# Kernel tuning notes

Hardware: AMD Instinct MI355X
Metric: run time of the kernel (lower is better)

The kernel has to match this reference:

```python
import jax, jax.numpy as jnp
import numpy as np

B, N, D = 4, 2048, 1024
HEAD_DIMS = 128
NUM_HEADS = 8
PROJ = HEAD_DIMS * NUM_HEADS  # 1024


def setup_inputs() -> dict:
    key = jax.random.key(0)
    ks = jax.random.split(key, 5)
    # Weights stored as (in, out); xavier-normal-like scale
    def xavier(k, fan_in, fan_out):
        std = (2.0 / (fan_in + fan_out)) ** 0.5
        return jax.random.normal(k, (fan_in, fan_out), dtype=jnp.float32) * std
    return {
        "x": jax.random.normal(ks[0], (B, N, D), dtype=jnp.float32),
        "Wq": xavier(ks[1], D, PROJ),
        "Wk": xavier(ks[2], D, PROJ),
        "Wv": xavier(ks[3], D, PROJ),
        "Wo": xavier(ks[4], PROJ, PROJ),
    }


def reference(x, Wq, Wk, Wv, Wo):
    b, n, d = x.shape
    # QKV projections, split into heads: (b, h, n, hd)
    def split_heads(z):
        return z.reshape(b, n, NUM_HEADS, HEAD_DIMS).transpose(0, 2, 1, 3)
    q = split_heads(x @ Wq)
    k = split_heads(x @ Wk)
    v = split_heads(x @ Wv)
    scale = 1.0 / jnp.sqrt(jnp.float32(HEAD_DIMS))
    logits = jnp.einsum("bhqd,bhkd->bhqk", q, k) * scale
    weights = jax.nn.softmax(logits, axis=-1)
    out = jnp.einsum("bhqk,bhkd->bhqd", weights, v)
    out = out.transpose(0, 2, 1, 3).reshape(b, n, PROJ)
    return out @ Wo
```

## Files before the change

kernel.cpp:

```cpp
#include <hip/hip_runtime.h>
#include <hip/hip_bf16.h>


typedef __attribute__((ext_vector_type(8))) short short8;
typedef __attribute__((ext_vector_type(4))) short short4v;
typedef __attribute__((ext_vector_type(4))) float floatx4;
typedef __attribute__((ext_vector_type(8))) _Float16 half8;

#define MFMA_F16(a, b, c) __builtin_amdgcn_mfma_f32_16x16x32_f16( \
    __builtin_bit_cast(half8, (a)), __builtin_bit_cast(half8, (b)), (c), 0, 0, 0)

static constexpr int BATCH  = 4;
static constexpr int NHEADS = 8;
static constexpr int SEQ    = 2048;
static constexpr int HD     = 128;
static constexpr int DMODEL = 1024;
static constexpr int MROWS  = BATCH * SEQ;
static constexpr int NQKV   = 3 * DMODEL;

#define QSCALE2 0.12752283786512624f

static __device__ __forceinline__ short f16bits(float v) {
    return __builtin_bit_cast(short, (_Float16)v);
}

template <typename T>
static __device__ __forceinline__ short8 load8_f16(const T* p) {
    if constexpr (sizeof(T) == 2) {
        return *(const short8*)p;
    } else {
        const float4 f0 = *(const float4*)p;
        const float4 f1 = *(const float4*)(p + 4);
        short8 r;
        r[0] = f16bits(f0.x); r[1] = f16bits(f0.y);
        r[2] = f16bits(f0.z); r[3] = f16bits(f0.w);
        r[4] = f16bits(f1.x); r[5] = f16bits(f1.y);
        r[6] = f16bits(f1.z); r[7] = f16bits(f1.w);
        return r;
    }
}

static __device__ __forceinline__ void storeC(float* C, size_t idx, float v) {
    C[idx] = v;
}
static __device__ __forceinline__ void storeC(_Float16* C, size_t idx, float v) {
    C[idx] = (_Float16)v;
}

static __device__ __forceinline__ void gload16(const short* g, short* l) {
    __builtin_amdgcn_global_load_lds(
        (const __attribute__((address_space(1))) void*)g,
        (__attribute__((address_space(3))) void*)l, 16, 0, 0);
}

__global__ __launch_bounds__(256)
void prep(const float* __restrict__ x, short* __restrict__ xb,
          const float* __restrict__ W0, const float* __restrict__ W1,
          const float* __restrict__ W2, const float* __restrict__ W3,
          short* __restrict__ Wt, int K, int N)
{
    __shared__ short T[32][33];
    const int z = blockIdx.z;
    if (z >= 4) {
        const size_t chunk = ((size_t)(z - 4) * 1024 + blockIdx.y * 32 + blockIdx.x);
        const size_t i = (chunk * 256 + threadIdx.x) * 8;
        *(short8*)&xb[i] = load8_f16(&x[i]);
        return;
    }
    const float* W = (z == 0) ? W0 : (z == 1) ? W1 : (z == 2) ? W2 : W3;
    short* Wtz = Wt + (size_t)z * K * N;

    const int n0 = blockIdx.x * 32, k0 = blockIdx.y * 32;
    const int r = threadIdx.x >> 3, c4 = (threadIdx.x & 7) * 4;

    const float4 v = *(const float4*)&W[(size_t)(k0 + r) * N + n0 + c4];
    T[r][c4 + 0] = f16bits(v.x);
    T[r][c4 + 1] = f16bits(v.y);
    T[r][c4 + 2] = f16bits(v.z);
    T[r][c4 + 3] = f16bits(v.w);
    __syncthreads();

    short4v o;
    o[0] = T[c4 + 0][r]; o[1] = T[c4 + 1][r];
    o[2] = T[c4 + 2][r]; o[3] = T[c4 + 3][r];
    *(short4v*)&Wtz[(size_t)(n0 + r) * K + k0 + c4] = o;
}

__global__ __launch_bounds__(256)
void convx(const float* __restrict__ x, short* __restrict__ xb)
{
    const size_t i = ((size_t)blockIdx.x * 256 + threadIdx.x) * 8;
    *(short8*)&xb[i] = load8_f16(&x[i]);
}

__global__ __launch_bounds__(256)
void transpose_v(const short* __restrict__ V, short* __restrict__ Vt)
{
    __shared__ short T[64][72];
    const int s0 = blockIdx.x * 64;
    const int d0 = blockIdx.y * 64;
    const int bh = blockIdx.z;
    const short* Vi = V  + (size_t)bh * SEQ * HD;
    short*       Vo = Vt + (size_t)bh * HD * SEQ;

    const int r = threadIdx.x >> 3;
    const int c = threadIdx.x & 7;

    *(short8*)&T[r][c * 8]      = *(const short8*)&Vi[(size_t)(s0 + r) * HD + d0 + c * 8];
    *(short8*)&T[r + 32][c * 8] = *(const short8*)&Vi[(size_t)(s0 + r + 32) * HD + d0 + c * 8];
    __syncthreads();

    short8 o0, o1;
    #pragma unroll
    for (int j = 0; j < 8; ++j) {
        o0[j] = T[c * 8 + j][r];
        o1[j] = T[c * 8 + j][r + 32];
    }
    *(short8*)&Vo[(size_t)(d0 + r) * SEQ + s0 + c * 8]      = o0;
    *(short8*)&Vo[(size_t)(d0 + r + 32) * SEQ + s0 + c * 8] = o1;
}

template <typename OutT, bool QKV>
__global__ __launch_bounds__(256)
void gemm128(const short* __restrict__ A, const short* __restrict__ Bt,
             OutT* __restrict__ C, int M, int N, int K, size_t qkvStride)
{
    __shared__ __align__(16) short As[128 * 64];
    __shared__ __align__(16) short Bs[128 * 64];

    const int tid  = threadIdx.x;
    const int lane = tid & 63;
    const int w    = tid >> 6;
    const int quad = lane >> 4;
    const int l16  = lane & 15;

    const int m0 = blockIdx.x * 128;
    const int n0 = blockIdx.y * 128;
    const int wm = (w >> 1) * 64;
    const int wn = (w & 1) * 64;

    floatx4 acc[4][4] = {};

    const int srow   = tid >> 3;
    const int schunk = (tid & 7) ^ (srow & 7);
    const short* aG = A  + (size_t)(m0 + srow) * K + schunk * 8;
    const short* bG = Bt + (size_t)(n0 + srow) * K + schunk * 8;
    short* aL = As + tid * 8;
    short* bL = Bs + tid * 8;

    const int fsw = l16 & 7;

    for (int k0 = 0; k0 < K; k0 += 64) {
        __syncthreads();
        #pragma unroll
        for (int r = 0; r < 4; ++r) {
            gload16(aG + k0 + (size_t)(r * 32) * K, aL + r * 2048);
            gload16(bG + k0 + (size_t)(r * 32) * K, bL + r * 2048);
        }
        __syncthreads();

        #pragma unroll
        for (int kk = 0; kk < 2; ++kk) {
            short8 af[4], bf[4];
            #pragma unroll
            for (int mi = 0; mi < 4; ++mi)
                af[mi] = *(short8*)&As[(wm + mi * 16 + l16) * 64 +
                                       (((kk * 4 + quad) ^ fsw) * 8)];
            #pragma unroll
            for (int ni = 0; ni < 4; ++ni)
                bf[ni] = *(short8*)&Bs[(wn + ni * 16 + l16) * 64 +
                                       (((kk * 4 + quad) ^ fsw) * 8)];

            #pragma unroll
            for (int mi = 0; mi < 4; ++mi)
                #pragma unroll
                for (int ni = 0; ni < 4; ++ni)
                    acc[mi][ni] = MFMA_F16(af[mi], bf[ni], acc[mi][ni]);
        }
    }

    #pragma unroll
    for (int mi = 0; mi < 4; ++mi)
        #pragma unroll
        for (int ni = 0; ni < 4; ++ni)
            #pragma unroll
            for (int r = 0; r < 4; ++r) {
                const int m = m0 + wm + mi * 16 + quad * 4 + r;
                const int n = n0 + wn + ni * 16 + l16;
                float v = acc[mi][ni][r];
                if constexpr (QKV) {
                    const int qkv = n >> 10, rem = n & 1023;
                    const int h = rem >> 7, d = rem & 127;
                    const int b = m >> 11, s = m & 2047;
                    if (qkv == 0) v *= QSCALE2;
                    storeC(C, (size_t)qkv * qkvStride +
                              (((size_t)b * NHEADS + h) * SEQ + s) * HD + d, v);
                } else {
                    storeC(C, (size_t)m * N + n, v);
                }
            }
}

__global__ __launch_bounds__(128)
void attn_flash12(const short* __restrict__ Q, const short* __restrict__ K,
                  const short* __restrict__ Vt, _Float16* __restrict__ O)
{
    __shared__ __align__(16) short Ks[2][32 * 128];
    __shared__ __align__(16) short Vs[2][128 * 32];
    __shared__ __align__(16) short Plds[2][32 * 40];

    const int tid  = threadIdx.x;
    const int lane = tid & 63;
    const int w    = tid >> 6;
    const int quad = lane >> 4;
    const int l16  = lane & 15;

    const int h  = blockIdx.x & 7;
    const int qi = blockIdx.x >> 3;
    const int b  = blockIdx.y;
    const int q0 = qi * 64;

    const short* Qh  = Q  + (((size_t)b * NHEADS + h) * SEQ) * HD;
    const short* Kh  = K  + (((size_t)b * NHEADS + h) * SEQ) * HD;
    const short* Vth = Vt + (((size_t)b * NHEADS + h) * HD) * SEQ;

    short8 qf[2][4];
    #pragma unroll
    for (int mi = 0; mi < 2; ++mi) {
        const int qrow = q0 + w * 32 + mi * 16 + l16;
        #pragma unroll
        for (int c = 0; c < 4; ++c)
            qf[mi][c] = *(const short8*)&Qh[(size_t)qrow * HD + c * 32 + quad * 8];
    }

    const int kr0 = tid >> 4, kc0 = tid & 15;
    const short* kA0 = Kh + (size_t)kr0 * HD + ((kc0 ^ kr0) * 8);
    const short* kA1 = Kh + (size_t)(kr0 + 8) * HD + ((kc0 ^ (kr0 + 8)) * 8);
    const int vr0 = tid >> 2, vp0 = tid & 3;
    const short* vA = Vth + (size_t)vr0 * SEQ + ((vp0 ^ ((vr0 >> 1) & 3)) * 8);

    floatx4 acc[2][8] = {};
    floatx4 acc9[2] = {};

    short8 ones;
    #pragma unroll
    for (int j = 0; j < 8; ++j) ones[j] = 0x3C00;

    const int fswV = (l16 >> 1) & 3;
    short* Pw = &Plds[w][0];

    auto STAGE_K = [&](short* dst, int tile) {
        const size_t ko = (size_t)tile * 32 * HD;
        gload16(kA0 + ko,           dst + tid * 8);
        gload16(kA1 + ko,           dst + (tid + 128) * 8);
        gload16(kA0 + ko + 16 * HD, dst + (tid + 256) * 8);
        gload16(kA1 + ko + 16 * HD, dst + (tid + 384) * 8);
    };
    auto STAGE_V = [&](short* dst, int tile) {
        const size_t vo = (size_t)tile * 32;
        gload16(vA + vo,                      dst + tid * 8);
        gload16(vA + vo + (size_t)32 * SEQ,   dst + (tid + 128) * 8);
        gload16(vA + vo + (size_t)64 * SEQ,   dst + (tid + 256) * 8);
        gload16(vA + vo + (size_t)96 * SEQ,   dst + (tid + 384) * 8);
    };

    auto QK = [&](const short* Kb, floatx4 (&s)[2][2]) {
        #pragma unroll
        for (int c = 0; c < 4; ++c) {
            const int k_ = c * 4 + quad;
            short8 kf0 = *(short8*)&Kb[l16 * 128 + ((k_ ^ l16) * 8)];
            short8 kf1 = *(short8*)&Kb[(16 + l16) * 128 + ((k_ ^ l16) * 8)];
            #pragma unroll
            for (int mi = 0; mi < 2; ++mi) {
                s[mi][0] = MFMA_F16(qf[mi][c], kf0, s[mi][0]);
                s[mi][1] = MFMA_F16(qf[mi][c], kf1, s[mi][1]);
            }
        }
    };

    auto ITER = [&](int T, int BB, floatx4 (&sin)[2][2], floatx4 (&sout)[2][2]) {
        __syncthreads();
        if (T + 2 < SEQ / 32) STAGE_K(&Ks[BB][0], T + 2);
        if (T + 1 < SEQ / 32) STAGE_V(&Vs[BB ^ 1][0], T + 1);

        #pragma unroll
        for (int mi = 0; mi < 2; ++mi)
            #pragma unroll
            for (int r = 0; r < 4; ++r) {
                const float p0 = __builtin_amdgcn_exp2f(sin[mi][0][r]);
                const float p1 = __builtin_amdgcn_exp2f(sin[mi][1][r]);
                const int prow = mi * 16 + quad * 4 + r;
                Pw[prow * 40 + l16]      = f16bits(p0);
                Pw[prow * 40 + 16 + l16] = f16bits(p1);
            }

        #pragma unroll
        for (int mi = 0; mi < 2; ++mi) {
            sout[mi][0] = floatx4{};
            sout[mi][1] = floatx4{};
        }
        if (T + 1 < SEQ / 32) QK(&Ks[BB ^ 1][0], sout);

        short8 pf[2];
        #pragma unroll
        for (int mi = 0; mi < 2; ++mi) {
            pf[mi] = *(short8*)&Pw[(mi * 16 + l16) * 40 + quad * 8];
            acc9[mi] = MFMA_F16(pf[mi], ones, acc9[mi]);
        }
        const short* Vb = &Vs[BB][0];
        #pragma unroll
        for (int hc = 0; hc < 8; ++hc) {
            short8 vf = *(short8*)&Vb[(hc * 16 + l16) * 32 + ((quad ^ fswV) * 8)];
            #pragma unroll
            for (int mi = 0; mi < 2; ++mi)
                acc[mi][hc] = MFMA_F16(pf[mi], vf, acc[mi][hc]);
        }
    };

    STAGE_K(&Ks[0][0], 0);
    STAGE_V(&Vs[0][0], 0);
    STAGE_K(&Ks[1][0], 1);
    __syncthreads();
    floatx4 sc[2][2] = {}, sn[2][2];
    QK(&Ks[0][0], sc);

    for (int t = 0; t < SEQ / 32; t += 2) {
        ITER(t,     0, sc, sn);
        ITER(t + 1, 1, sn, sc);
    }

    #pragma unroll
    for (int mi = 0; mi < 2; ++mi) {
        float rinv[4];
        #pragma unroll
        for (int r = 0; r < 4; ++r)
            rinv[r] = 1.0f / fmaxf(acc9[mi][r], 1e-30f);
        #pragma unroll
        for (int hc = 0; hc < 8; ++hc)
            #pragma unroll
            for (int r = 0; r < 4; ++r) {
                const int row = q0 + w * 32 + mi * 16 + quad * 4 + r;
                O[((size_t)b * SEQ + row) * DMODEL + h * HD + hc * 16 + l16] =
                    (_Float16)(acc[mi][hc][r] * rinv[r]);
            }
    }
}

template <typename AT, typename OutT>
__global__ __launch_bounds__(256)
void gemm64(const AT* __restrict__ A, const float* __restrict__ W,
            OutT* __restrict__ C, int M, int N, int K, int headsplit)
{
    __shared__ __align__(16) short As[64][32];
    __shared__ __align__(16) short Bs[64][32];

    const int tid  = threadIdx.x;
    const int lane = tid & 63;
    const int w    = tid >> 6;
    const int quad = lane >> 4;
    const int l16  = lane & 15;

    const int m0 = blockIdx.x * 64;
    const int n0 = blockIdx.y * 64;
    const int wm = (w >> 1) * 32;
    const int wn = (w & 1) * 32;

    floatx4 acc[2][2] = {};

    const int arow = tid >> 2, acol = (tid & 3) * 8;
    const int brow = tid >> 3, bcol = (tid & 7) * 8;

    const AT*    aptr = A + (size_t)(m0 + arow) * K + acol;
    const float* bptr = W + (size_t)brow * N + n0 + bcol;

    for (int k0 = 0; k0 < K; k0 += 32) {
        short8 av = load8_f16(aptr + k0);
        short8 bv = load8_f16(bptr + (size_t)k0 * N);
        __syncthreads();
        *(short8*)&As[arow][acol] = av;
        #pragma unroll
        for (int j = 0; j < 8; ++j)
            Bs[bcol + j][brow] = bv[j];
        __syncthreads();

        short8 af0 = *(short8*)&As[wm + l16][quad * 8];
        short8 af1 = *(short8*)&As[wm + 16 + l16][quad * 8];
        short8 bf0 = *(short8*)&Bs[wn + l16][quad * 8];
        short8 bf1 = *(short8*)&Bs[wn + 16 + l16][quad * 8];

        acc[0][0] = MFMA_F16(af0, bf0, acc[0][0]);
        acc[0][1] = MFMA_F16(af0, bf1, acc[0][1]);
        acc[1][0] = MFMA_F16(af1, bf0, acc[1][0]);
        acc[1][1] = MFMA_F16(af1, bf1, acc[1][1]);
    }

    #pragma unroll
    for (int mi = 0; mi < 2; ++mi)
        #pragma unroll
        for (int ni = 0; ni < 2; ++ni)
            #pragma unroll
            for (int r = 0; r < 4; ++r) {
                const int m = m0 + wm + mi * 16 + quad * 4 + r;
                const int n = n0 + wn + ni * 16 + l16;
                const float v = acc[mi][ni][r];
                if (headsplit) {
                    const int b = m >> 11, nn = m & 2047;
                    const int h = n >> 7,  d  = n & 127;
                    storeC(C, (((size_t)b * NHEADS + h) * SEQ + nn) * HD + d, v);
                } else {
                    storeC(C, (size_t)m * N + n, v);
                }
            }
}

__global__ __launch_bounds__(256)
void attn_flash(const short* __restrict__ Q, const short* __restrict__ K,
                const short* __restrict__ V, _Float16* __restrict__ O)
{
    __shared__ __align__(16) short Ksf[32][136];
    __shared__ __align__(16) short Vtl[HD][40];
    __shared__ __align__(16) short Pldsf[4][16][40];

    const int tid  = threadIdx.x;
    const int lane = tid & 63;
    const int w    = tid >> 6;
    const int quad = lane >> 4;
    const int l16  = lane & 15;

    const int q0 = blockIdx.x * 64;
    const int h  = blockIdx.y;
    const int b  = blockIdx.z;

    const size_t headoff = ((size_t)b * NHEADS + h) * SEQ * HD;
    const short* Qh = Q + headoff;
    const short* Kh = K + headoff;
    const short* Vh = V + headoff;

    const float scale = 0.08838834764831845f;

    const int qrow = q0 + w * 16 + l16;
    short8 qf[4];
    #pragma unroll
    for (int c = 0; c < 4; ++c)
        qf[c] = *(const short8*)&Qh[(size_t)qrow * HD + c * 32 + quad * 8];

    float mrow[4], lrow[4];
    #pragma unroll
    for (int r = 0; r < 4; ++r) { mrow[r] = -1e30f; lrow[r] = 0.f; }
    floatx4 acc[8] = {};

    const int krow = tid >> 4, kcol = (tid & 15) * 8;
    const int vkey = tid & 31;
    const int vhd  = (tid >> 5) * 16;

    for (int kt = 0; kt < SEQ; kt += 32) {
        const short* Kt = Kh + (size_t)kt * HD;
        short8 k0v = *(const short8*)(Kt + (size_t)tid * 8);
        short8 k1v = *(const short8*)(Kt + (size_t)(tid + 256) * 8);
        short8 v0 = *(const short8*)&Vh[(size_t)(kt + vkey) * HD + vhd];
        short8 v1 = *(const short8*)&Vh[(size_t)(kt + vkey) * HD + vhd + 8];

        __syncthreads();
        *(short8*)&Ksf[krow][kcol]      = k0v;
        *(short8*)&Ksf[krow + 16][kcol] = k1v;
        #pragma unroll
        for (int j = 0; j < 8; ++j) {
            Vtl[vhd + j][vkey]     = v0[j];
            Vtl[vhd + 8 + j][vkey] = v1[j];
        }
        __syncthreads();

        floatx4 s0 = {}, s1 = {};
        #pragma unroll
        for (int c = 0; c < 4; ++c) {
            short8 kf0 = *(short8*)&Ksf[l16][c * 32 + quad * 8];
            short8 kf1 = *(short8*)&Ksf[16 + l16][c * 32 + quad * 8];
            s0 = MFMA_F16(qf[c], kf0, s0);
            s1 = MFMA_F16(qf[c], kf1, s1);
        }

        float p0[4], p1[4], alpha[4];
        #pragma unroll
        for (int r = 0; r < 4; ++r) {
            const float a  = s0[r] * scale;
            const float bb = s1[r] * scale;
            float mx = fmaxf(a, bb);
            mx = fmaxf(mx, __shfl_xor(mx, 1));
            mx = fmaxf(mx, __shfl_xor(mx, 2));
            mx = fmaxf(mx, __shfl_xor(mx, 4));
            mx = fmaxf(mx, __shfl_xor(mx, 8));
            const float mnew = fmaxf(mrow[r], mx);
            alpha[r] = __expf(mrow[r] - mnew);
            mrow[r]  = mnew;
            p0[r] = __expf(a - mnew);
            p1[r] = __expf(bb - mnew);
            float rs = p0[r] + p1[r];
            rs += __shfl_xor(rs, 1);
            rs += __shfl_xor(rs, 2);
            rs += __shfl_xor(rs, 4);
            rs += __shfl_xor(rs, 8);
            lrow[r] = lrow[r] * alpha[r] + rs;
        }
        #pragma unroll
        for (int hc = 0; hc < 8; ++hc)
            #pragma unroll
            for (int r = 0; r < 4; ++r)
                acc[hc][r] *= alpha[r];

        #pragma unroll
        for (int r = 0; r < 4; ++r) {
            Pldsf[w][quad * 4 + r][l16]      = f16bits(p0[r]);
            Pldsf[w][quad * 4 + r][16 + l16] = f16bits(p1[r]);
        }
        __syncthreads();

        short8 pf = *(short8*)&Pldsf[w][l16][quad * 8];
        #pragma unroll
        for (int hc = 0; hc < 8; ++hc) {
            short8 vf = *(short8*)&Vtl[hc * 16 + l16][quad * 8];
            acc[hc] = MFMA_F16(pf, vf, acc[hc]);
        }
    }

    #pragma unroll
    for (int hc = 0; hc < 8; ++hc)
        #pragma unroll
        for (int r = 0; r < 4; ++r) {
            const int row = q0 + w * 16 + quad * 4 + r;
            const float val = acc[hc][r] / fmaxf(lrow[r], 1e-30f);
            O[((size_t)b * SEQ + row) * DMODEL + h * HD + hc * 16 + l16] =
                (_Float16)val;
        }
}

extern "C" void kernel_launch(void* const* d_in, const int* in_sizes, int n_in,
                              void* d_out, int out_size, void* d_ws, size_t ws_size,
                              hipStream_t stream)
{
    const float* x  = (const float*)d_in[0];
    const float* Wq = (const float*)d_in[1];
    const float* Wk = (const float*)d_in[2];
    const float* Wv = (const float*)d_in[3];
    const float* Wo = (const float*)d_in[4];
    float* out = (float*)d_out;

    const size_t bufElems = (size_t)MROWS * DMODEL;
    const size_t batElems = (size_t)SEQ * DMODEL;
    const size_t MiB = 1024 * 1024;
    dim3 tt(256);
    dim3 ta(128);

    if (ws_size >= 72 * MiB) {
        short* xb    = (short*)d_ws;
        short* Qb    = xb + bufElems;
        short* Kb    = xb + 2 * bufElems;
        short* Vn    = xb + 3 * bufElems;
        short* Wtall = xb + 4 * bufElems;
        short* Wto   = Wtall + 3 * (size_t)DMODEL * DMODEL;
        short* VtG   = xb;
        short* Ab    = Vn;

        prep<<<dim3(32, 32, 8), tt, 0, stream>>>(
            x, xb, Wq, Wk, Wv, Wo, Wtall, DMODEL, DMODEL);

        gemm128<_Float16, true><<<dim3(MROWS / 128, NQKV / 128), tt, 0, stream>>>(
            xb, Wtall, (_Float16*)Qb, MROWS, NQKV, DMODEL, bufElems);

        transpose_v<<<dim3(SEQ / 64, HD / 64, BATCH * NHEADS), tt, 0, stream>>>(Vn, VtG);

        attn_flash12<<<dim3(NHEADS * (SEQ / 64), BATCH), ta, 0, stream>>>(
            Qb, Kb, VtG, (_Float16*)Ab);

        gemm128<float, false><<<dim3(MROWS / 128, DMODEL / 128), tt, 0, stream>>>(
            Ab, Wto, out, MROWS, DMODEL, DMODEL, 0);
    } else if (ws_size >= 64 * MiB) {
        short* xb    = (short*)d_ws;
        short* Qb    = xb + 2 * batElems;
        short* Kb    = Qb + 4 * batElems;
        short* Vn    = Kb + 4 * batElems;
        short* Wtall = Vn + 4 * batElems;
        short* Wto   = Wtall + 3 * (size_t)DMODEL * DMODEL;

        prep<<<dim3(32, 32, 4), tt, 0, stream>>>(
            nullptr, nullptr, Wq, Wk, Wv, Wo, Wtall, DMODEL, DMODEL);

        for (int half = 0; half < 2; ++half) {
            const size_t off = (size_t)half * 2 * batElems;
            convx<<<dim3(2048), tt, 0, stream>>>(x + off, xb);
            gemm128<_Float16, true><<<dim3(32, NQKV / 128), tt, 0, stream>>>(
                xb, Wtall, (_Float16*)(Qb + off), 2 * SEQ, NQKV, DMODEL,
                4 * batElems);
        }
        for (int half = 0; half < 2; ++half) {
            const size_t off = (size_t)half * 2 * batElems;
            transpose_v<<<dim3(SEQ / 64, HD / 64, 2 * NHEADS), tt, 0, stream>>>(
                Vn + off, xb);
            attn_flash12<<<dim3(NHEADS * (SEQ / 64), 2), ta, 0, stream>>>(
                Qb + off, Kb + off, xb, (_Float16*)(Vn + off));
        }
        gemm128<float, false><<<dim3(MROWS / 128, DMODEL / 128), tt, 0, stream>>>(
            Vn, Wto, out, MROWS, DMODEL, DMODEL, 0);
    } else if (ws_size >= 24 * MiB) {
        short* xb    = (short*)d_ws;
        short* Qb    = xb + batElems;
        short* Kb    = xb + 2 * batElems;
        short* Vb    = xb + 3 * batElems;
        short* Wtall = xb + 4 * batElems;
        short* Wto   = Wtall + 3 * (size_t)DMODEL * DMODEL;

        prep<<<dim3(32, 32, 4), tt, 0, stream>>>(
            nullptr, nullptr, Wq, Wk, Wv, Wo, Wtall, DMODEL, DMODEL);

        for (int b = 0; b < BATCH; ++b) {
            convx<<<dim3(1024), tt, 0, stream>>>(x + (size_t)b * batElems, xb);
            gemm128<_Float16, true><<<dim3(SEQ / 128, NQKV / 128), tt, 0, stream>>>(
                xb, Wtall, (_Float16*)Qb, SEQ, NQKV, DMODEL, batElems);
            transpose_v<<<dim3(SEQ / 64, HD / 64, NHEADS), tt, 0, stream>>>(Vb, xb);
            attn_flash12<<<dim3(NHEADS * (SEQ / 64), 1), ta, 0, stream>>>(
                Qb, Kb, xb, (_Float16*)Vb);
            gemm128<float, false><<<dim3(SEQ / 128, DMODEL / 128), tt, 0, stream>>>(
                Vb, Wto, out + (size_t)b * batElems, SEQ, DMODEL, DMODEL, 0);
        }
    } else {
        short* Qb = (short*)d_ws;
        short* Kb = Qb + batElems;
        short* Vb = Qb + 2 * batElems;
        short* Ab = Qb + 3 * batElems;

        dim3 gg(SEQ / 64, DMODEL / 64);
        for (int b = 0; b < BATCH; ++b) {
            const float* xb_ = x + (size_t)b * batElems;
            gemm64<float, _Float16><<<gg, tt, 0, stream>>>(
                xb_, Wq, (_Float16*)Qb, SEQ, DMODEL, DMODEL, 1);
            gemm64<float, _Float16><<<gg, tt, 0, stream>>>(
                xb_, Wk, (_Float16*)Kb, SEQ, DMODEL, DMODEL, 1);
            gemm64<float, _Float16><<<gg, tt, 0, stream>>>(
                xb_, Wv, (_Float16*)Vb, SEQ, DMODEL, DMODEL, 1);
            attn_flash<<<dim3(SEQ / 64, NHEADS, 1), tt, 0, stream>>>(
                Qb, Kb, Vb, (_Float16*)Ab);
            gemm64<short, float><<<gg, tt, 0, stream>>>(
                Ab, Wo, out + (size_t)b * batElems, SEQ, DMODEL, DMODEL, 0);
        }
    }
}
```

Before: 292.3 us.

## Keep softmax P in registers via transposed QK MFMA, drop LDS round-trip

Swaps the operand order of the QK^T MFMA so each lane's score accumulator already matches the A-operand layout needed for the PV MFMA. The exp2 results are then packed to f16 with cvt_pkrtz straight into registers, which removes the per-warp P staging buffer in shared memory and its LDS writes and reads. To keep the k-index ordering consistent, the V fragment is now assembled from two 4-element LDS reads. It also raises wave priority around the MFMA blocks. The cost is extra LDS read instructions for V, plus round-toward-zero conversion instead of round-to-nearest.

After: 323.8 us. 10.8% more time.

```diff
diff --git a/kernel.cpp b/kernel.cpp
--- a/kernel.cpp
+++ b/kernel.cpp
@@ -6,6 +6,7 @@
 typedef __attribute__((ext_vector_type(4))) short short4v;
 typedef __attribute__((ext_vector_type(4))) float floatx4;
 typedef __attribute__((ext_vector_type(8))) _Float16 half8;
+typedef __attribute__((ext_vector_type(4))) unsigned uint4v;
 
 #define MFMA_F16(a, b, c) __builtin_amdgcn_mfma_f32_16x16x32_f16( \
     __builtin_bit_cast(half8, (a)), __builtin_bit_cast(half8, (b)), (c), 0, 0, 0)
@@ -22,6 +23,11 @@
 
 static __device__ __forceinline__ short f16bits(float v) {
     return __builtin_bit_cast(short, (_Float16)v);
+}
+
+static __device__ __forceinline__ unsigned pk2(float a, float b) {
+    auto h = __builtin_amdgcn_cvt_pkrtz(a, b);
+    return __builtin_bit_cast(unsigned, h);
 }
 
 template <typename T>
@@ -202,12 +208,11 @@
 }
 
 __global__ __launch_bounds__(128)
-void attn_flash12(const short* __restrict__ Q, const short* __restrict__ K,
+void attn_flash13(const short* __restrict__ Q, const short* __restrict__ K,
                   const short* __restrict__ Vt, _Float16* __restrict__ O)
 {
     __shared__ __align__(16) short Ks[2][32 * 128];
     __shared__ __align__(16) short Vs[2][128 * 32];
-    __shared__ __align__(16) short Plds[2][32 * 40];
 
     const int tid  = threadIdx.x;
     const int lane = tid & 63;
@@ -247,7 +252,6 @@
     for (int j = 0; j < 8; ++j) ones[j] = 0x3C00;
 
     const int fswV = (l16 >> 1) & 3;
-    short* Pw = &Plds[w][0];
 
     auto STAGE_K = [&](short* dst, int tile) {
         const size_t ko = (size_t)tile * 32 * HD;
@@ -265,6 +269,7 @@
     };
 
     auto QK = [&](const short* Kb, floatx4 (&s)[2][2]) {
+        __builtin_amdgcn_s_setprio(1);
         #pragma unroll
         for (int c = 0; c < 4; ++c) {
             const int k_ = c * 4 + quad;
@@ -272,10 +277,11 @@
             short8 kf1 = *(short8*)&Kb[(16 + l16) * 128 + ((k_ ^ l16) * 8)];
             #pragma unroll
             for (int mi = 0; mi < 2; ++mi) {
-                s[mi][0] = MFMA_F16(qf[mi][c], kf0, s[mi][0]);
-                s[mi][1] = MFMA_F16(qf[mi][c], kf1, s[mi][1]);
+                s[mi][0] = MFMA_F16(kf0, qf[mi][c], s[mi][0]);
+                s[mi][1] = MFMA_F16(kf1, qf[mi][c], s[mi][1]);
             }
         }
+        __builtin_amdgcn_s_setprio(0);
     };
 
     auto ITER = [&](int T, int BB, floatx4 (&sin)[2][2], floatx4 (&sout)[2][2]) {
@@ -283,16 +289,20 @@
         if (T + 2 < SEQ / 32) STAGE_K(&Ks[BB][0], T + 2);
         if (T + 1 < SEQ / 32) STAGE_V(&Vs[BB ^ 1][0], T + 1);
 
-        #pragma unroll
-        for (int mi = 0; mi < 2; ++mi)
-            #pragma unroll
-            for (int r = 0; r < 4; ++r) {
-                const float p0 = __builtin_amdgcn_exp2f(sin[mi][0][r]);
-                const float p1 = __builtin_amdgcn_exp2f(sin[mi][1][r]);
-                const int prow = mi * 16 + quad * 4 + r;
-                Pw[prow * 40 + l16]      = f16bits(p0);
-                Pw[prow * 40 + 16 + l16] = f16bits(p1);
-            }
+        short8 pf[2];
+        #pragma unroll
+        for (int mi = 0; mi < 2; ++mi) {
+            uint4v pw;
+            pw[0] = pk2(__builtin_amdgcn_exp2f(sin[mi][0][0]),
+                        __builtin_amdgcn_exp2f(sin[mi][0][1]));
+            pw[1] = pk2(__builtin_amdgcn_exp2f(sin[mi][0][2]),
+                        __builtin_amdgcn_exp2f(sin[mi][0][3]));
+            pw[2] = pk2(__builtin_amdgcn_exp2f(sin[mi][1][0]),
+                        __builtin_amdgcn_exp2f(sin[mi][1][1]));
+            pw[3] = pk2(__builtin_amdgcn_exp2f(sin[mi][1][2]),
+                        __builtin_amdgcn_exp2f(sin[mi][1][3]));
+            pf[mi] = __builtin_bit_cast(short8, pw);
+        }
 
         #pragma unroll
         for (int mi = 0; mi < 2; ++mi) {
@@ -301,20 +311,25 @@
         }
         if (T + 1 < SEQ / 32) QK(&Ks[BB ^ 1][0], sout);
 
-        short8 pf[2];
-        #pragma unroll
-        for (int mi = 0; mi < 2; ++mi) {
-            pf[mi] = *(short8*)&Pw[(mi * 16 + l16) * 40 + quad * 8];
+        #pragma unroll
+        for (int mi = 0; mi < 2; ++mi)
             acc9[mi] = MFMA_F16(pf[mi], ones, acc9[mi]);
-        }
+
         const short* Vb = &Vs[BB][0];
+        __builtin_amdgcn_s_setprio(1);
         #pragma unroll
         for (int hc = 0; hc < 8; ++hc) {
-            short8 vf = *(short8*)&Vb[(hc * 16 + l16) * 32 + ((quad ^ fswV) * 8)];
+            const int vbase = (hc * 16 + l16) * 32 + (quad & 1) * 4;
+            short4v vlo = *(short4v*)&Vb[vbase + (((quad >> 1)    ) ^ fswV) * 8];
+            short4v vhi = *(short4v*)&Vb[vbase + (((quad >> 1) + 2) ^ fswV) * 8];
+            short8 vf;
+            vf[0] = vlo[0]; vf[1] = vlo[1]; vf[2] = vlo[2]; vf[3] = vlo[3];
+            vf[4] = vhi[0]; vf[5] = vhi[1]; vf[6] = vhi[2]; vf[7] = vhi[3];
             #pragma unroll
             for (int mi = 0; mi < 2; ++mi)
                 acc[mi][hc] = MFMA_F16(pf[mi], vf, acc[mi][hc]);
         }
+        __builtin_amdgcn_s_setprio(0);
     };
 
     STAGE_K(&Ks[0][0], 0);
@@ -568,7 +583,7 @@
 
         transpose_v<<<dim3(SEQ / 64, HD / 64, BATCH * NHEADS), tt, 0, stream>>>(Vn, VtG);
 
-        attn_flash12<<<dim3(NHEADS * (SEQ / 64), BATCH), ta, 0, stream>>>(
+        attn_flash13<<<dim3(NHEADS * (SEQ / 64), BATCH), ta, 0, stream>>>(
             Qb, Kb, VtG, (_Float16*)Ab);
 
         gemm128<float, false><<<dim3(MROWS / 128, DMODEL / 128), tt, 0, stream>>>(
@@ -595,7 +610,7 @@
             const size_t off = (size_t)half * 2 * batElems;
             transpose_v<<<dim3(SEQ / 64, HD / 64, 2 * NHEADS), tt, 0, stream>>>(
                 Vn + off, xb);
-            attn_flash12<<<dim3(NHEADS * (SEQ / 64), 2), ta, 0, stream>>>(
+            attn_flash13<<<dim3(NHEADS * (SEQ / 64), 2), ta, 0, stream>>>(
                 Qb + off, Kb + off, xb, (_Float16*)(Vn + off));
         }
         gemm128<float, false><<<dim3(MROWS / 128, DMODEL / 128), tt, 0, stream>>>(
@@ -616,7 +631,7 @@
             gemm128<_Float16, true><<<dim3(SEQ / 128, NQKV / 128), tt, 0, stream>>>(
                 xb, Wtall, (_Float16*)Qb, SEQ, NQKV, DMODEL, batElems);
             transpose_v<<<dim3(SEQ / 64, HD / 64, NHEADS), tt, 0, stream>>>(Vb, xb);
-            attn_flash12<<<dim3(NHEADS * (SEQ / 64), 1), ta, 0, stream>>>(
+            attn_flash13<<<dim3(NHEADS * (SEQ / 64), 1), ta, 0, stream>>>(
                 Qb, Kb, xb, (_Float16*)Vb);
             gemm128<float, false><<<dim3(SEQ / 128, DMODEL / 128), tt, 0, stream>>>(
                 Vb, Wto, out + (size_t)b * batElems, SEQ, DMODEL, DMODEL, 0);
```
